# Optimization experiments

Measured on AMD Instinct MI355X. Metric: run time of the kernel, lower is better.

The kernel has to match this reference:

```python
import jax, jax.numpy as jnp
import numpy as np

B, S, E, H, DH, F, L, C = 32, 197, 768, 12, 64, 2048, 4, 1000
LN_EPS = 1e-5


def setup_inputs() -> dict:
    key = jax.random.key(0)
    ks = jax.random.split(key, 16)
    sc = 0.02
    return {
        "x": jax.random.normal(ks[0], (B, S, E), dtype=jnp.float32),
        "Wk": jax.random.normal(ks[1], (L, H, E, DH), dtype=jnp.float32) * sc,
        "Wq": jax.random.normal(ks[2], (L, H, E, DH), dtype=jnp.float32) * sc,
        "Wv": jax.random.normal(ks[3], (L, H, E, DH), dtype=jnp.float32) * sc,
        "Wconv": jax.random.normal(ks[4], (L, H * DH, E), dtype=jnp.float32) * sc,
        "ln1_w": jnp.ones((L, E), jnp.float32),
        "ln1_b": jnp.zeros((L, E), jnp.float32),
        "ln2_w": jnp.ones((L, E), jnp.float32),
        "ln2_b": jnp.zeros((L, E), jnp.float32),
        "W1": jax.random.normal(ks[5], (L, E, F), dtype=jnp.float32) * sc,
        "b1": jnp.zeros((L, F), jnp.float32),
        "W2": jax.random.normal(ks[6], (L, F, E), dtype=jnp.float32) * sc,
        "b2": jnp.zeros((L, E), jnp.float32),
        "Wc": jax.random.normal(ks[7], (E, C), dtype=jnp.float32) * sc,
        "bc": jnp.zeros((C,), jnp.float32),
    }


def _layernorm(x, w, b):
    mu = jnp.mean(x, axis=-1, keepdims=True)
    var = jnp.mean(jnp.square(x - mu), axis=-1, keepdims=True)
    return (x - mu) * jax.lax.rsqrt(var + LN_EPS) * w + b


def reference(x, Wk, Wq, Wv, Wconv, ln1_w, ln1_b, ln2_w, ln2_b, W1, b1, W2, b2, Wc, bc):
    # NOTE: original scales attention scores by sqrt(seq_len), not sqrt(d_k)
    seq_len = x.shape[1]
    inv_scale = 1.0 / jnp.sqrt(jnp.float32(seq_len))
    h = x
    for l in range(L):  # small fixed layer loop
        xn = _layernorm(h, ln1_w[l], ln1_b[l])
        q = jnp.einsum('bse,hed->bhsd', xn, Wq[l])
        k = jnp.einsum('bse,hed->bhsd', xn, Wk[l])
        v = jnp.einsum('bse,hed->bhsd', xn, Wv[l])
        scores = jnp.einsum('bhsd,bhtd->bhst', q, k) * inv_scale
        att = jax.nn.softmax(scores, axis=-1)
        o = jnp.einsum('bhst,bhtd->bhsd', att, v)
        # concat heads: b s (h d), head index outermost in last dim
        o = o.transpose(0, 2, 1, 3).reshape(o.shape[0], o.shape[2], H * DH)
        mha = o @ Wconv[l]
        res1 = mha + h
        xn2 = _layernorm(res1, ln2_w[l], ln2_b[l])
        ff = jax.nn.gelu(xn2 @ W1[l] + b1[l], approximate=False) @ W2[l] + b2[l]
        h = ff + res1
    logits = h[:, 0] @ Wc + bc
    return jax.nn.softmax(logits, axis=-1)
```

## Files before the change

kernel.cpp:

```cpp
#include <hip/hip_runtime.h>
#include <hip/hip_bf16.h>
#include <math.h>

#define BQ 32
#define SQ 197
#define EQ 768
#define HQ 12
#define DHQ 64
#define FQ 2048
#define LQ 4
#define CQ 1000
#define BSQ (BQ*SQ)
#define SP 208
#define S16 13
#define MP (BQ*SP)
#define QKV3 2304
#define KTP 7
#define LN_EPS 1e-5f

typedef __bf16 bf16x8 __attribute__((ext_vector_type(8)));
typedef float f32x4 __attribute__((ext_vector_type(4)));
typedef unsigned short u16x8 __attribute__((ext_vector_type(8)));

typedef const __attribute__((address_space(1))) unsigned int* gas_t;
typedef __attribute__((address_space(3))) unsigned int* las_t;

__device__ __forceinline__ __hip_bfloat16 tobf(float f) { return __float2bfloat16(f); }

__device__ __forceinline__ size_t pk(int rt, int KT, int kt, int lane) {
    return (((size_t)rt * KT + kt) * 64 + (size_t)lane) * 8;
}

#define QPK_SLAB (S16*2*512)
#define QPK_TOT  ((size_t)BQ*HQ*QPK_SLAB + 4096)
#define VPK_SLAB (4*KTP*512)
#define VPK_TOT  ((size_t)BQ*HQ*VPK_SLAB + 4096)

template<int N>
__device__ __forceinline__ void waitvm() {
    asm volatile("s_waitcnt vmcnt(%0)" :: "n"(N) : "memory");
}
__device__ __forceinline__ void barx() {
    asm volatile("" ::: "memory");
    __builtin_amdgcn_s_barrier();
    asm volatile("" ::: "memory");
}
__device__ __forceinline__ void lds_fence() {
    asm volatile("s_waitcnt lgkmcnt(0)" ::: "memory");
    __builtin_amdgcn_sched_barrier(0);
}

__device__ __forceinline__ float gelu_f(float v) {
    float ax = fabsf(v) * 0.70710678118654752f;
    float t  = __builtin_amdgcn_rcpf(1.0f + 0.3275911f * ax);
    float p  = ((((1.061405429f * t - 1.453152027f) * t + 1.421413741f) * t
               - 0.284496736f) * t + 0.254829592f) * t;
    float e  = __expf(-ax * ax);
    float er = 1.0f - p * e;
    return v * (0.5f * (1.0f + copysignf(er, v)));
}

__global__ __launch_bounds__(256) void copy_pad(const float* __restrict__ x,
    float* __restrict__ bh)
{
    int r = blockIdx.x;
    int b = r / SQ, s = r % SQ;
    const float* src = x + (size_t)r * EQ;
    float* dst = bh + ((size_t)b * SP + s) * EQ;
    int t = threadIdx.x;
    dst[t] = src[t];
    dst[t + 256] = src[t + 256];
    dst[t + 512] = src[t + 512];
}

__device__ __forceinline__ void tconv_body(const float* __restrict__ ip,
    unsigned short* __restrict__ out, int C, int KT, int ntb_base, int r0, int c0)
{
    __shared__ float tile[64][65];
    int t = threadIdx.x;
    int tc = t & 63, tr = t >> 6;
    #pragma unroll
    for (int p = 0; p < 16; ++p) {
        int r = p * 4 + tr;
        tile[r][tc] = ip[(size_t)(r0 + r) * C + c0 + tc];
    }
    __syncthreads();
    int ntb = ntb_base + (c0 >> 4);
    int ktb = r0 >> 5;
    #pragma unroll
    for (int p = 0; p < 2; ++p) {
        int cc = p * 256 + t;
        int lane = cc & 63, grp = cc >> 6;
        int ktl = grp & 1, ntl = grp >> 1;
        int er = ktl * 32 + (lane >> 4) * 8;
        int dc = ntl * 16 + (lane & 15);
        u16x8 v;
        #pragma unroll
        for (int e = 0; e < 8; ++e) {
            __hip_bfloat16 h = tobf(tile[er + e][dc]);
            v[e] = *(unsigned short*)&h;
        }
        *(u16x8*)(out + pk(ntb + ntl, KT, ktb + ktl, lane)) = v;
    }
}

__global__ __launch_bounds__(256) void tconv_pk(const float* __restrict__ in,
    unsigned short* __restrict__ out, int C, int KT, size_t slab, int ntPerSlab)
{
    tconv_body(in + (size_t)blockIdx.z * slab, out, C, KT,
               blockIdx.z * ntPerSlab, blockIdx.x * 64, blockIdx.y * 64);
}

__global__ __launch_bounds__(256) void tconv_qkv3(const float* __restrict__ Wq,
    const float* __restrict__ Wk, const float* __restrict__ Wv,
    unsigned short* __restrict__ out)
{
    int z = blockIdx.z;
    int which = z / HQ, zz = z - which * HQ;
    const float* src = (which == 0) ? Wq : (which == 1) ? Wk : Wv;
    tconv_body(src + (size_t)zz * EQ * DHQ, out + (size_t)which * EQ * EQ,
               DHQ, 24, zz * 4, blockIdx.x * 64, 0);
}

__global__ __launch_bounds__(256) void ln_kernel(const float* __restrict__ in,
    const float* __restrict__ w, const float* __restrict__ b,
    __hip_bfloat16* __restrict__ out)
{
    int row = blockIdx.x;
    const float* x = in + (size_t)row * EQ;
    int t = threadIdx.x;
    float v0 = x[t];
    float v1 = x[t + 256];
    float v2 = x[t + 512];
    __shared__ float red[256];
    red[t] = v0 + v1 + v2;
    __syncthreads();
    for (int off = 128; off > 0; off >>= 1) {
        if (t < off) red[t] += red[t + off];
        __syncthreads();
    }
    float mu = red[0] * (1.0f / EQ);
    __syncthreads();
    float d0 = v0 - mu, d1 = v1 - mu, d2 = v2 - mu;
    red[t] = d0*d0 + d1*d1 + d2*d2;
    __syncthreads();
    for (int off = 128; off > 0; off >>= 1) {
        if (t < off) red[t] += red[t + off];
        __syncthreads();
    }
    float rs = rsqrtf(red[0] * (1.0f / EQ) + LN_EPS);
    int rt = row >> 4, rsl = row & 15;
    float n0 = d0 * rs * w[t]       + b[t];
    float n1 = d1 * rs * w[t + 256] + b[t + 256];
    float n2 = d2 * rs * w[t + 512] + b[t + 512];
    #pragma unroll
    for (int p = 0; p < 3; ++p) {
        int k = t + (p << 8);
        float val = p == 0 ? n0 : (p == 1 ? n1 : n2);
        int kt = k >> 5, lane = (((k >> 3) & 3) << 4) + rsl, e = k & 7;
        out[pk(rt, 24, kt, lane) + e] = tobf(val);
    }
}

template<int KT, int RT>
__device__ __forceinline__ void kloop_staged(
    const unsigned short* __restrict__ Apk,
    const unsigned short* __restrict__ Bpk,
    int rtb, int ntb, int tid, unsigned short* sm, f32x4 (&acc)[RT][4])
{
    static_assert(KT >= 3, "need >=3 k-tiles");
    constexpr int AC  = RT * 2;
    constexpr int NCH = AC + 8;
    constexpr int CPW = NCH / 4;
    const int lane = tid & 63, w = tid >> 6;
    const int wr = w >> 1, wc = w & 1;
    const int cbase = w * CPW;

    const unsigned short* sp[CPW];
    #pragma unroll
    for (int q = 0; q < CPW; ++q) {
        int c = cbase + q;
        sp[q] = (c < AC) ? Apk + pk(rtb + c, KT, 0, lane)
                         : Bpk + pk(ntb + (c - AC), KT, 0, lane);
    }
    unsigned short* bufs0 = sm;
    unsigned short* bufs1 = sm + NCH * 512;
    unsigned short* bufs2 = sm + 2 * NCH * 512;

    auto stagef = [&](unsigned short* dst) {
        #pragma unroll
        for (int q = 0; q < CPW; ++q) {
            __builtin_amdgcn_global_load_lds(
                (gas_t)sp[q], (las_t)(dst + (cbase + q) * 512), 16, 0, 0);
            sp[q] += 512;
        }
    };
    auto frags = [&](const unsigned short* cur, bf16x8 (&af)[RT], bf16x8 (&bb)[4]) {
        #pragma unroll
        for (int i = 0; i < RT; ++i)
            af[i] = *(const bf16x8*)(cur + (wr * RT + i) * 512 + lane * 8);
        #pragma unroll
        for (int j = 0; j < 4; ++j)
            bb[j] = *(const bf16x8*)(cur + (AC + wc * 4 + j) * 512 + lane * 8);
    };
    auto mf = [&](bf16x8 (&af)[RT], bf16x8 (&bb)[4]) {
        #pragma unroll
        for (int i = 0; i < RT; ++i)
            #pragma unroll
            for (int j = 0; j < 4; ++j)
                acc[i][j] = __builtin_amdgcn_mfma_f32_16x16x32_bf16(af[i], bb[j], acc[i][j], 0, 0, 0);
    };

    stagef(bufs0);
    stagef(bufs1);
    unsigned short *cur = bufs0, *nxt = bufs1, *nx2 = bufs2;

    #pragma unroll 1
    for (int kt = 0; kt < KT - 2; ++kt) {
        waitvm<CPW>();
        barx();
        bf16x8 af[RT], bb[4];
        frags(cur, af, bb);
        stagef(nx2);
        mf(af, bb);
        unsigned short* t_ = cur; cur = nxt; nxt = nx2; nx2 = t_;
    }
    {
        waitvm<CPW>();
        barx();
        bf16x8 af[RT], bb[4];
        frags(cur, af, bb);
        mf(af, bb);
        cur = nxt;
    }
    {
        waitvm<0>();
        barx();
        bf16x8 af[RT], bb[4];
        frags(cur, af, bb);
        mf(af, bb);
    }
}

enum { EPI_NONE = 0, EPI_RES = 1, EPI_BIAS_GELU = 2, EPI_BIAS_RES = 3, EPI_QKV = 4 };

template<int EPI, int KT, int RT>
__global__ __launch_bounds__(256, 3) void mgemm_pk(
    const unsigned short* __restrict__ Apk, const unsigned short* __restrict__ Bpk,
    void* __restrict__ Cm, const float* __restrict__ bias,
    const float* __restrict__ res, int N, int nNT)
{
    constexpr int NCH = RT * 2 + 8;
    __shared__ __align__(16) unsigned short smem[(3 * NCH * 1024) / 2];

    const int nRowT = (RT == 4) ? 52 : 104;
    const int g = blockIdx.x & 7;
    const int sIdx = blockIdx.x >> 3;
    const int b0 = (nRowT * g) >> 3, b1 = (nRowT * (g + 1)) >> 3;
    const int colT = sIdx % nNT, rloc = sIdx / nNT;
    if (b0 + rloc >= b1) return;
    const int row0 = (b0 + rloc) * (RT * 32), col0 = colT << 7;

    const int tid = threadIdx.x;
    const int lane = tid & 63;
    const int w = tid >> 6;
    const int wr = w >> 1, wc = w & 1;
    const int l15 = lane & 15, quad = lane >> 4;

    f32x4 acc[RT][4] = {};
    kloop_staged<KT, RT>(Apk, Bpk, row0 >> 4, col0 >> 4, tid, smem, acc);

    if constexpr (EPI == EPI_BIAS_GELU) {
        __syncthreads();
        auto Cs = (unsigned short (*)[136])smem;
        #pragma unroll
        for (int j = 0; j < 4; ++j) {
            float bv = bias[col0 + wc * 64 + j * 16 + l15];
            #pragma unroll
            for (int i = 0; i < RT; ++i)
                #pragma unroll
                for (int rg = 0; rg < 4; ++rg) {
                    float v = gelu_f(acc[i][j][rg] + bv);
                    __hip_bfloat16 h = tobf(v);
                    Cs[wr * 64 + i * 16 + quad * 4 + rg][wc * 64 + j * 16 + l15] =
                        *(unsigned short*)&h;
                }
        }
        __syncthreads();
        const int KT2 = N >> 5;
        #pragma unroll
        for (int p = 0; p < 8; ++p) {
            int cc = p * 256 + tid;
            int ln2 = cc & 63, grp = cc >> 6;
            int ktl = grp & 3, rtl = grp >> 2;
            int rowl = rtl * 16 + (ln2 & 15);
            u16x8 v;
            #pragma unroll
            for (int e = 0; e < 8; ++e)
                v[e] = Cs[rowl][ktl * 32 + (ln2 >> 4) * 8 + e];
            *(u16x8*)((unsigned short*)Cm + pk((row0 >> 4) + rtl, KT2, (col0 >> 5) + ktl, ln2)) = v;
        }
    } else if constexpr (EPI == EPI_QKV) {
        unsigned short* qpk = (unsigned short*)Cm;
        unsigned short* kpk = (unsigned short*)(void*)bias;
        unsigned short* vpk = (unsigned short*)(void*)res;
        __syncthreads();
        auto Cs = (unsigned short (*)[136])smem;
        #pragma unroll
        for (int j = 0; j < 4; ++j)
            #pragma unroll
            for (int i = 0; i < 4; ++i)
                #pragma unroll
                for (int rg = 0; rg < 4; ++rg) {
                    __hip_bfloat16 h = tobf(acc[i][j][rg]);
                    Cs[wr * 64 + i * 16 + quad * 4 + rg][wc * 64 + j * 16 + l15] =
                        *(unsigned short*)&h;
                }
        __syncthreads();

        const int treg = col0 >> 7;
        if (treg < 12) {
            unsigned short* dst = (treg < 6) ? qpk : kpk;
            const int h0 = ((col0 % 768) >> 6);
            #pragma unroll
            for (int p = 0; p < 8; ++p) {
                int cc = p * 256 + tid;
                int ln2 = cc & 63, grp = cc >> 6;
                int hl = grp & 1, kt = (grp >> 1) & 1, rtl = grp >> 2;
                int row16 = (row0 >> 4) + rtl;
                int bb = row16 / S16;
                int s16 = row16 - bb * S16;
                int h = h0 + hl;
                u16x8 v;
                #pragma unroll
                for (int e = 0; e < 8; ++e)
                    v[e] = Cs[rtl * 16 + (ln2 & 15)][hl * 64 + kt * 32 + (ln2 >> 4) * 8 + e];
                *(u16x8*)(dst + ((((size_t)(bb * HQ + h) * S16 + s16) * 2 + kt) << 9) + ln2 * 8) = v;
            }
        } else {
            const int h0 = (col0 - 1536) >> 6;
            #pragma unroll
            for (int p = 0; p < 8; ++p) {
                int cc = p * 256 + tid;
                int dloc = cc & 127;
                int g8 = cc >> 7;
                int gr = row0 + g8 * 8;
                int bb = gr / SP;
                int tl = gr - bb * SP;
                int tt = tl >> 5;
                int tsub = (tl >> 3) & 3;
                int h = h0 + (dloc >> 6);
                int dt = (dloc >> 4) & 3;
                int lane2 = tsub * 16 + (dloc & 15);
                u16x8 v;
                #pragma unroll
                for (int e = 0; e < 8; ++e)
                    v[e] = Cs[g8 * 8 + e][dloc];
                *(u16x8*)(vpk + (size_t)(bb * HQ + h) * VPK_SLAB + pk(dt, KTP, tt, lane2)) = v;
            }
        }
    } else {
        #pragma unroll
        for (int j = 0; j < 4; ++j) {
            int c = col0 + wc * 64 + j * 16 + l15;
            float bv = (EPI == EPI_BIAS_RES) ? bias[c] : 0.f;
            #pragma unroll
            for (int i = 0; i < RT; ++i)
                #pragma unroll
                for (int rg = 0; rg < 4; ++rg) {
                    int r = row0 + wr * (RT * 16) + i * 16 + quad * 4 + rg;
                    float v = acc[i][j][rg];
                    size_t idx = (size_t)r * N + c;
                    if (EPI == EPI_BIAS_RES) {
                        ((float*)Cm)[idx] = v + bv + res[idx];
                    } else if (EPI == EPI_RES) {
                        ((float*)Cm)[idx] = v + res[idx];
                    } else {
                        ((__hip_bfloat16*)Cm)[idx] = tobf(v);
                    }
                }
        }
    }
}

__global__ __launch_bounds__(128, 4) void attn_fused(
    const unsigned short* __restrict__ qpk, const unsigned short* __restrict__ kpk,
    const unsigned short* __restrict__ vpk, unsigned short* __restrict__ opk)
{
    __shared__ unsigned short Ps[2][16][240];
    __shared__ unsigned short Cs[2][16][72];
    const int bh = blockIdx.x;
    const int b = bh / HQ, h = bh - b * HQ;
    const int tid = threadIdx.x;
    const int w = tid >> 6, lane = tid & 63;
    const int l15 = lane & 15, quad = lane >> 4;
    const int rt = blockIdx.y * 2 + w;
    if (rt >= S16) return;

    const unsigned short* qs = qpk + (size_t)bh * QPK_SLAB;
    const unsigned short* ks = kpk + (size_t)bh * QPK_SLAB;
    const unsigned short* vs = vpk + (size_t)bh * VPK_SLAB;

    bf16x8 af0 = *(const bf16x8*)(qs + ((rt * 2 + 0) << 9) + lane * 8);
    bf16x8 af1 = *(const bf16x8*)(qs + ((rt * 2 + 1) << 9) + lane * 8);

    f32x4 acc[13] = {};
    bf16x8 kc0 = *(const bf16x8*)(ks + (0 << 9) + lane * 8);
    bf16x8 kc1 = *(const bf16x8*)(ks + (1 << 9) + lane * 8);
    #pragma unroll
    for (int j = 0; j < 13; ++j) {
        bf16x8 kn0, kn1;
        if (j + 1 < 13) {
            kn0 = *(const bf16x8*)(ks + (((j + 1) * 2 + 0) << 9) + lane * 8);
            kn1 = *(const bf16x8*)(ks + (((j + 1) * 2 + 1) << 9) + lane * 8);
        }
        __builtin_amdgcn_s_setprio(1);
        acc[j] = __builtin_amdgcn_mfma_f32_16x16x32_bf16(af0, kc0, acc[j], 0, 0, 0);
        acc[j] = __builtin_amdgcn_mfma_f32_16x16x32_bf16(af1, kc1, acc[j], 0, 0, 0);
        __builtin_amdgcn_s_setprio(0);
        kc0 = kn0; kc1 = kn1;
    }

    bf16x8 vb[4];
    #pragma unroll
    for (int d = 0; d < 4; ++d)
        vb[d] = *(const bf16x8*)(vs + pk(d, KTP, 0, lane));

    const float scale = 0.07124704998790965f;
    const int xr = (quad & 2) << 3;
    const unsigned short zbf = 0;
    float inv[4];
    #pragma unroll
    for (int rg = 0; rg < 4; ++rg) {
        float y[13];
        float m = -1e30f;
        #pragma unroll
        for (int j = 0; j < 13; ++j) {
            float v = acc[j][rg] * scale;
            if (j == 12) v = (l15 < 5) ? v : -1e30f;
            y[j] = v;
            m = fmaxf(m, v);
        }
        #pragma unroll
        for (int d = 1; d < 16; d <<= 1) m = fmaxf(m, __shfl_xor(m, d));
        float s = 0.f;
        #pragma unroll
        for (int j = 0; j < 13; ++j) {
            float e = __expf(y[j] - m);
            s += e;
            __hip_bfloat16 hv = tobf(e);
            Ps[w][quad * 4 + rg][(j * 16 + l15) ^ xr] = *(unsigned short*)&hv;
        }
        Ps[w][quad * 4 + rg][(208 + l15) ^ xr] = zbf;
        #pragma unroll
        for (int d = 1; d < 16; d <<= 1) s += __shfl_xor(s, d);
        inv[rg] = 1.0f / s;
    }
    lds_fence();

    f32x4 av[4] = {};
    #pragma unroll
    for (int kk = 0; kk < KTP; ++kk) {
        bf16x8 vn[4];
        if (kk + 1 < KTP) {
            #pragma unroll
            for (int d = 0; d < 4; ++d)
                vn[d] = *(const bf16x8*)(vs + pk(d, KTP, kk + 1, lane));
        }
        int col = (kk * 32 + quad * 8) ^ ((l15 & 8) << 1);
        bf16x8 pf = *(const bf16x8*)&Ps[w][l15][col];
        __builtin_amdgcn_s_setprio(1);
        #pragma unroll
        for (int d = 0; d < 4; ++d)
            av[d] = __builtin_amdgcn_mfma_f32_16x16x32_bf16(pf, vb[d], av[d], 0, 0, 0);
        __builtin_amdgcn_s_setprio(0);
        #pragma unroll
        for (int d = 0; d < 4; ++d) vb[d] = vn[d];
    }

    #pragma unroll
    for (int d = 0; d < 4; ++d)
        #pragma unroll
        for (int rg = 0; rg < 4; ++rg) {
            __hip_bfloat16 hv = tobf(av[d][rg] * inv[rg]);
            Cs[w][quad * 4 + rg][d * 16 + l15] = *(unsigned short*)&hv;
        }
    lds_fence();

    const int rtg = b * S16 + rt;
    #pragma unroll
    for (int ktl = 0; ktl < 2; ++ktl) {
        u16x8 v;
        #pragma unroll
        for (int e = 0; e < 8; ++e)
            v[e] = Cs[w][l15][ktl * 32 + quad * 8 + e];
        *(u16x8*)(opk + pk(rtg, 24, h * 2 + ktl, lane)) = v;
    }
}

__global__ __launch_bounds__(256) void logits_kernel(
    const float* __restrict__ hbuf, const float* __restrict__ Wc,
    const float* __restrict__ bc, float* __restrict__ logits)
{
    __shared__ __align__(16) float hs[768];
    __shared__ float red[256];
    int b = blockIdx.y;
    int tid = threadIdx.x;
    const float* hr = hbuf + (size_t)b * SP * EQ;
    for (int p = tid; p < 192; p += 256)
        *(float4*)&hs[p << 2] = *(const float4*)(hr + (p << 2));
    __syncthreads();
    int cl = tid & 31, ks = tid >> 5;
    int c = blockIdx.x * 32 + cl;
    int cs = (c < CQ) ? c : 0;
    float s = 0.f;
    int e0 = ks * 96;
    #pragma unroll 8
    for (int e = 0; e < 96; ++e)
        s = fmaf(hs[e0 + e], Wc[(size_t)(e0 + e) * CQ + cs], s);
    red[tid] = s;
    __syncthreads();
    for (int off = 128; off >= 32; off >>= 1) {
        if (tid < off) red[tid] += red[tid + off];
        __syncthreads();
    }
    if (tid < 32 && c < CQ)
        logits[(size_t)b * CQ + c] = red[tid] + bc[c];
}

__global__ __launch_bounds__(256) void smax_kernel(
    const float* __restrict__ logits, float* __restrict__ out)
{
    __shared__ float red[256];
    int b = blockIdx.x;
    int t = threadIdx.x;
    const float* lp = logits + (size_t)b * CQ;
    float lg[4];
    #pragma unroll
    for (int j = 0; j < 4; ++j) {
        int c = t + j * 256;
        lg[j] = (c < CQ) ? lp[c] : -1e30f;
    }
    float m = fmaxf(fmaxf(lg[0], lg[1]), fmaxf(lg[2], lg[3]));
    red[t] = m;
    __syncthreads();
    for (int off = 128; off; off >>= 1) {
        if (t < off) red[t] = fmaxf(red[t], red[t + off]);
        __syncthreads();
    }
    m = red[0];
    __syncthreads();
    float ex[4], s = 0.f;
    #pragma unroll
    for (int j = 0; j < 4; ++j) {
        ex[j] = (t + j * 256 < CQ) ? __expf(lg[j] - m) : 0.f;
        s += ex[j];
    }
    red[t] = s;
    __syncthreads();
    for (int off = 128; off; off >>= 1) {
        if (t < off) red[t] += red[t + off];
        __syncthreads();
    }
    float inv = 1.0f / red[0];
    #pragma unroll
    for (int j = 0; j < 4; ++j)
        if (t + j * 256 < CQ) out[(size_t)b * CQ + t + j * 256] = ex[j] * inv;
}

extern "C" void kernel_launch(void* const* d_in, const int* in_sizes, int n_in,
                              void* d_out, int out_size, void* d_ws, size_t ws_size,
                              hipStream_t stream)
{
    const float* x     = (const float*)d_in[0];
    const float* Wk    = (const float*)d_in[1];
    const float* Wq    = (const float*)d_in[2];
    const float* Wv    = (const float*)d_in[3];
    const float* Wconv = (const float*)d_in[4];
    const float* ln1w  = (const float*)d_in[5];
    const float* ln1b  = (const float*)d_in[6];
    const float* ln2w  = (const float*)d_in[7];
    const float* ln2b  = (const float*)d_in[8];
    const float* W1    = (const float*)d_in[9];
    const float* b1    = (const float*)d_in[10];
    const float* W2    = (const float*)d_in[11];
    const float* b2    = (const float*)d_in[12];
    const float* Wc    = (const float*)d_in[13];
    const float* bc    = (const float*)d_in[14];
    float* out = (float*)d_out;

    const size_t MPE = (size_t)MP * EQ;

    float* w = (float*)d_ws;
    float* bh    = w; w += MPE;
    float* res1  = w; w += MPE;
    float* logit = w; w += (size_t)BQ * CQ;
    unsigned short* qpk  = (unsigned short*)w;
    unsigned short* kpk  = qpk + QPK_TOT;
    unsigned short* vpk  = kpk + QPK_TOT;
    unsigned short* actb = vpk + VPK_TOT;
    unsigned short* ffh  = actb + MPE;
    unsigned short* wbuf = ffh + (size_t)MP * FQ;

    const size_t WQKV = (size_t)EQ * EQ;
    unsigned short* WcvT = wbuf;
    unsigned short* W1T  = wbuf + WQKV;
    unsigned short* W2T  = W1T + (size_t)EQ * FQ;

    copy_pad<<<BSQ, 256, 0, stream>>>(x, bh);

    for (int l = 0; l < LQ; ++l) {
        tconv_qkv3<<<dim3(12, 1, 3 * HQ), 256, 0, stream>>>(
            Wq + (size_t)l * HQ * EQ * DHQ, Wk + (size_t)l * HQ * EQ * DHQ,
            Wv + (size_t)l * HQ * EQ * DHQ, wbuf);

        ln_kernel<<<MP, 256, 0, stream>>>(bh, ln1w + l * EQ, ln1b + l * EQ, (__hip_bfloat16*)actb);

        mgemm_pk<EPI_QKV, 24, 4><<<8 * 7 * 18, 256, 0, stream>>>(
            actb, wbuf, qpk, (const float*)kpk, (const float*)vpk, QKV3, 18);

        tconv_pk<<<dim3(12, 12, 1), 256, 0, stream>>>(Wconv + (size_t)l * EQ * EQ, WcvT, EQ, 24, 0, 0);
        tconv_pk<<<dim3(12, 32, 1), 256, 0, stream>>>(W1 + (size_t)l * EQ * FQ, W1T, FQ, 24, 0, 0);
        tconv_pk<<<dim3(32, 12, 1), 256, 0, stream>>>(W2 + (size_t)l * FQ * EQ, W2T, EQ, 64, 0, 0);

        attn_fused<<<dim3(BQ * HQ, 7), 128, 0, stream>>>(qpk, kpk, vpk, actb);

        mgemm_pk<EPI_RES, 24, 2><<<8 * 13 * 6, 256, 0, stream>>>(
            actb, WcvT, res1, nullptr, bh, EQ, 6);

        ln_kernel<<<MP, 256, 0, stream>>>(res1, ln2w + l * EQ, ln2b + l * EQ, (__hip_bfloat16*)actb);

        mgemm_pk<EPI_BIAS_GELU, 24, 4><<<8 * 7 * 16, 256, 0, stream>>>(
            actb, W1T, ffh, b1 + l * FQ, nullptr, FQ, 16);
        mgemm_pk<EPI_BIAS_RES, 64, 2><<<8 * 13 * 6, 256, 0, stream>>>(
            ffh, W2T, bh, b2 + l * EQ, res1, EQ, 6);
    }
    logits_kernel<<<dim3(32, BQ), 256, 0, stream>>>(bh, Wc, bc, logit);
    smax_kernel<<<BQ, 256, 0, stream>>>(logit, out);
}
```

Before: 793.8 us.

## Batch weight conversions into one launch and use wave-per-row layernorm

Replaces the four per-layer weight transpose/convert launches with a single upfront kernel that converts every layer's weights into a per-layer slab. This cuts the launch count and lets the conversions run with full-GPU parallelism. The layernorm kernel now handles one row per wavefront, using vector loads and shuffle reductions instead of block-wide shared-memory reductions with many barriers. copy_pad now also zero-fills the padding rows, and the workspace grows to hold bf16 weights for all layers.

```diff
diff --git a/kernel.cpp b/kernel.cpp
--- a/kernel.cpp
+++ b/kernel.cpp
@@ -35,6 +35,7 @@
 #define QPK_TOT  ((size_t)BQ*HQ*QPK_SLAB + 4096)
 #define VPK_SLAB (4*KTP*512)
 #define VPK_TOT  ((size_t)BQ*HQ*VPK_SLAB + 4096)
+#define LWSLAB (4*(size_t)EQ*EQ + 2*(size_t)EQ*FQ)
 
 template<int N>
 __device__ __forceinline__ void waitvm() {
@@ -64,13 +65,17 @@
     float* __restrict__ bh)
 {
     int r = blockIdx.x;
-    int b = r / SQ, s = r % SQ;
-    const float* src = x + (size_t)r * EQ;
-    float* dst = bh + ((size_t)b * SP + s) * EQ;
+    int b = r / SP, s = r - b * SP;
+    float* dst = bh + (size_t)r * EQ;
     int t = threadIdx.x;
-    dst[t] = src[t];
-    dst[t + 256] = src[t + 256];
-    dst[t + 512] = src[t + 512];
+    if (s < SQ) {
+        const float* src = x + ((size_t)b * SQ + s) * EQ;
+        dst[t]       = src[t];
+        dst[t + 256] = src[t + 256];
+        dst[t + 512] = src[t + 512];
+    } else {
+        dst[t] = 0.f; dst[t + 256] = 0.f; dst[t + 512] = 0.f;
+    }
 }
 
 __device__ __forceinline__ void tconv_body(const float* __restrict__ ip,
@@ -104,62 +109,92 @@
     }
 }
 
-__global__ __launch_bounds__(256) void tconv_pk(const float* __restrict__ in,
-    unsigned short* __restrict__ out, int C, int KT, size_t slab, int ntPerSlab)
-{
-    tconv_body(in + (size_t)blockIdx.z * slab, out, C, KT,
-               blockIdx.z * ntPerSlab, blockIdx.x * 64, blockIdx.y * 64);
-}
-
-__global__ __launch_bounds__(256) void tconv_qkv3(const float* __restrict__ Wq,
-    const float* __restrict__ Wk, const float* __restrict__ Wv,
-    unsigned short* __restrict__ out)
-{
-    int z = blockIdx.z;
-    int which = z / HQ, zz = z - which * HQ;
-    const float* src = (which == 0) ? Wq : (which == 1) ? Wk : Wv;
-    tconv_body(src + (size_t)zz * EQ * DHQ, out + (size_t)which * EQ * EQ,
-               DHQ, 24, zz * 4, blockIdx.x * 64, 0);
+__global__ __launch_bounds__(256) void tconv_all(
+    const float* __restrict__ Wq, const float* __restrict__ Wk,
+    const float* __restrict__ Wv, const float* __restrict__ Wcv,
+    const float* __restrict__ W1, const float* __restrict__ W2,
+    unsigned short* __restrict__ wAll)
+{
+    int id = blockIdx.x;
+    const int l = id / 1344; id -= l * 1344;
+    unsigned short* wl = wAll + (size_t)l * LWSLAB;
+    const float* src; unsigned short* dst;
+    int C, KT, ntb, r0, c0;
+    if (id < 432) {
+        int x = id % 12, z = id / 12;
+        int which = z / 12, zz = z - which * 12;
+        const float* s0 = (which == 0) ? Wq : (which == 1) ? Wk : Wv;
+        src = s0 + ((size_t)l * HQ + zz) * EQ * DHQ;
+        dst = wl + (size_t)which * EQ * EQ;
+        C = DHQ; KT = 24; ntb = zz * 4; r0 = x * 64; c0 = 0;
+    } else if (id < 576) {
+        int t = id - 432;
+        src = Wcv + (size_t)l * EQ * EQ;
+        dst = wl + 3 * (size_t)EQ * EQ;
+        C = EQ; KT = 24; ntb = 0; r0 = (t % 12) * 64; c0 = (t / 12) * 64;
+    } else if (id < 960) {
+        int t = id - 576;
+        src = W1 + (size_t)l * EQ * FQ;
+        dst = wl + 4 * (size_t)EQ * EQ;
+        C = FQ; KT = 24; ntb = 0; r0 = (t % 12) * 64; c0 = (t / 12) * 64;
+    } else {
+        int t = id - 960;
+        src = W2 + (size_t)l * FQ * EQ;
+        dst = wl + 4 * (size_t)EQ * EQ + (size_t)EQ * FQ;
+        C = EQ; KT = 64; ntb = 0; r0 = (t % 32) * 64; c0 = (t / 32) * 64;
+    }
+    tconv_body(src, dst, C, KT, ntb, r0, c0);
 }
 
 __global__ __launch_bounds__(256) void ln_kernel(const float* __restrict__ in,
     const float* __restrict__ w, const float* __restrict__ b,
-    __hip_bfloat16* __restrict__ out)
-{
-    int row = blockIdx.x;
+    unsigned short* __restrict__ out)
+{
+    const int wv = threadIdx.x >> 6, L = threadIdx.x & 63;
+    const int row = blockIdx.x * 4 + wv;
     const float* x = in + (size_t)row * EQ;
-    int t = threadIdx.x;
-    float v0 = x[t];
-    float v1 = x[t + 256];
-    float v2 = x[t + 512];
-    __shared__ float red[256];
-    red[t] = v0 + v1 + v2;
-    __syncthreads();
-    for (int off = 128; off > 0; off >>= 1) {
-        if (t < off) red[t] += red[t + off];
-        __syncthreads();
-    }
-    float mu = red[0] * (1.0f / EQ);
-    __syncthreads();
-    float d0 = v0 - mu, d1 = v1 - mu, d2 = v2 - mu;
-    red[t] = d0*d0 + d1*d1 + d2*d2;
-    __syncthreads();
-    for (int off = 128; off > 0; off >>= 1) {
-        if (t < off) red[t] += red[t + off];
-        __syncthreads();
-    }
-    float rs = rsqrtf(red[0] * (1.0f / EQ) + LN_EPS);
-    int rt = row >> 4, rsl = row & 15;
-    float n0 = d0 * rs * w[t]       + b[t];
-    float n1 = d1 * rs * w[t + 256] + b[t + 256];
-    float n2 = d2 * rs * w[t + 512] + b[t + 512];
-    #pragma unroll
-    for (int p = 0; p < 3; ++p) {
-        int k = t + (p << 8);
-        float val = p == 0 ? n0 : (p == 1 ? n1 : n2);
-        int kt = k >> 5, lane = (((k >> 3) & 3) << 4) + rsl, e = k & 7;
-        out[pk(rt, 24, kt, lane) + e] = tobf(val);
-    }
+    float4 a0 = *(const float4*)(x + 8 * L);
+    float4 a1 = *(const float4*)(x + 8 * L + 4);
+    float4 a2 = make_float4(0.f, 0.f, 0.f, 0.f), a3 = a2;
+    const bool two = (L < 32);
+    if (two) {
+        a2 = *(const float4*)(x + 512 + 8 * L);
+        a3 = *(const float4*)(x + 512 + 8 * L + 4);
+    }
+    float s = a0.x + a0.y + a0.z + a0.w + a1.x + a1.y + a1.z + a1.w
+            + a2.x + a2.y + a2.z + a2.w + a3.x + a3.y + a3.z + a3.w;
+    #pragma unroll
+    for (int d = 1; d < 64; d <<= 1) s += __shfl_xor(s, d);
+    const float mu = s * (1.0f / EQ);
+    float q = (a0.x-mu)*(a0.x-mu) + (a0.y-mu)*(a0.y-mu) + (a0.z-mu)*(a0.z-mu) + (a0.w-mu)*(a0.w-mu)
+            + (a1.x-mu)*(a1.x-mu) + (a1.y-mu)*(a1.y-mu) + (a1.z-mu)*(a1.z-mu) + (a1.w-mu)*(a1.w-mu);
+    if (two)
+        q += (a2.x-mu)*(a2.x-mu) + (a2.y-mu)*(a2.y-mu) + (a2.z-mu)*(a2.z-mu) + (a2.w-mu)*(a2.w-mu)
+           + (a3.x-mu)*(a3.x-mu) + (a3.y-mu)*(a3.y-mu) + (a3.z-mu)*(a3.z-mu) + (a3.w-mu)*(a3.w-mu);
+    #pragma unroll
+    for (int d = 1; d < 64; d <<= 1) q += __shfl_xor(q, d);
+    const float rs = rsqrtf(q * (1.0f / EQ) + LN_EPS);
+
+    const int rt = row >> 4, rsl = row & 15;
+    auto store_chunk = [&](int c, float4 v0, float4 v1) {
+        int kt = c >> 2, c2 = c & 3;
+        int lane2 = (c2 << 4) + rsl;
+        int k0 = c << 3;
+        float4 w0 = *(const float4*)(w + k0), w1 = *(const float4*)(w + k0 + 4);
+        float4 g0 = *(const float4*)(b + k0), g1 = *(const float4*)(b + k0 + 4);
+        float va[8] = {v0.x, v0.y, v0.z, v0.w, v1.x, v1.y, v1.z, v1.w};
+        float wa[8] = {w0.x, w0.y, w0.z, w0.w, w1.x, w1.y, w1.z, w1.w};
+        float ba[8] = {g0.x, g0.y, g0.z, g0.w, g1.x, g1.y, g1.z, g1.w};
+        u16x8 o;
+        #pragma unroll
+        for (int e = 0; e < 8; ++e) {
+            __hip_bfloat16 h = tobf((va[e] - mu) * rs * wa[e] + ba[e]);
+            o[e] = *(unsigned short*)&h;
+        }
+        *(u16x8*)(out + pk(rt, 24, kt, lane2)) = o;
+    };
+    store_chunk(L, a0, a1);
+    if (two) store_chunk(64 + L, a2, a3);
 }
 
 template<int KT, int RT>
@@ -600,35 +635,28 @@
     unsigned short* vpk  = kpk + QPK_TOT;
     unsigned short* actb = vpk + VPK_TOT;
     unsigned short* ffh  = actb + MPE;
-    unsigned short* wbuf = ffh + (size_t)MP * FQ;
-
-    const size_t WQKV = (size_t)EQ * EQ;
-    unsigned short* WcvT = wbuf;
-    unsigned short* W1T  = wbuf + WQKV;
-    unsigned short* W2T  = W1T + (size_t)EQ * FQ;
-
-    copy_pad<<<BSQ, 256, 0, stream>>>(x, bh);
+    unsigned short* wAll = ffh + (size_t)MP * FQ;
+
+    copy_pad<<<MP, 256, 0, stream>>>(x, bh);
+    tconv_all<<<4 * 1344, 256, 0, stream>>>(Wq, Wk, Wv, Wconv, W1, W2, wAll);
 
     for (int l = 0; l < LQ; ++l) {
-        tconv_qkv3<<<dim3(12, 1, 3 * HQ), 256, 0, stream>>>(
-            Wq + (size_t)l * HQ * EQ * DHQ, Wk + (size_t)l * HQ * EQ * DHQ,
-            Wv + (size_t)l * HQ * EQ * DHQ, wbuf);
-
-        ln_kernel<<<MP, 256, 0, stream>>>(bh, ln1w + l * EQ, ln1b + l * EQ, (__hip_bfloat16*)actb);
+        unsigned short* wl   = wAll + (size_t)l * LWSLAB;
+        unsigned short* WcvT = wl + 3 * (size_t)EQ * EQ;
+        unsigned short* W1T  = wl + 4 * (size_t)EQ * EQ;
+        unsigned short* W2T  = W1T + (size_t)EQ * FQ;
+
+        ln_kernel<<<MP / 4, 256, 0, stream>>>(bh, ln1w + l * EQ, ln1b + l * EQ, actb);
 
         mgemm_pk<EPI_QKV, 24, 4><<<8 * 7 * 18, 256, 0, stream>>>(
-            actb, wbuf, qpk, (const float*)kpk, (const float*)vpk, QKV3, 18);
-
-        tconv_pk<<<dim3(12, 12, 1), 256, 0, stream>>>(Wconv + (size_t)l * EQ * EQ, WcvT, EQ, 24, 0, 0);
-        tconv_pk<<<dim3(12, 32, 1), 256, 0, stream>>>(W1 + (size_t)l * EQ * FQ, W1T, FQ, 24, 0, 0);
-        tconv_pk<<<dim3(32, 12, 1), 256, 0, stream>>>(W2 + (size_t)l * FQ * EQ, W2T, EQ, 64, 0, 0);
+            actb, wl, qpk, (const float*)kpk, (const float*)vpk, QKV3, 18);
 
         attn_fused<<<dim3(BQ * HQ, 7), 128, 0, stream>>>(qpk, kpk, vpk, actb);
 
         mgemm_pk<EPI_RES, 24, 2><<<8 * 13 * 6, 256, 0, stream>>>(
             actb, WcvT, res1, nullptr, bh, EQ, 6);
 
-        ln_kernel<<<MP, 256, 0, stream>>>(res1, ln2w + l * EQ, ln2b + l * EQ, (__hip_bfloat16*)actb);
+        ln_kernel<<<MP / 4, 256, 0, stream>>>(res1, ln2w + l * EQ, ln2b + l * EQ, actb);
 
         mgemm_pk<EPI_BIAS_GELU, 24, 4><<<8 * 7 * 16, 256, 0, stream>>>(
             actb, W1T, ffh, b1 + l * FQ, nullptr, FQ, 16);
```

After: 710.5 us. 10.5% less time.
